# Kernel tuning notes

Hardware: AMD Instinct MI355X
Metric: run time of the kernel (lower is better)

Reference implementation:

```python
import jax, jax.numpy as jnp
import numpy as np

NUM_EMBEDDINGS = 8192
EMBEDDING_DIM = 128


def setup_inputs() -> dict:
    key = jax.random.key(0)
    k1, k2 = jax.random.split(key)
    inputs = jax.random.normal(k1, (8, 32, 32, EMBEDDING_DIM), dtype=jnp.float32)
    embedding_weight = jax.random.normal(k2, (NUM_EMBEDDINGS, EMBEDDING_DIM), dtype=jnp.float32)
    return {"inputs": inputs, "embedding_weight": embedding_weight}


def reference(inputs, embedding_weight):
    # inputs: [B, H, W, C] channels-last; embedding_weight: [K, C]
    input_shape = inputs.shape
    flat_input = inputs.reshape(-1, EMBEDDING_DIM)  # [N, C]

    distances = (
        jnp.sum(flat_input ** 2, axis=1, keepdims=True)
        + jnp.sum(embedding_weight ** 2, axis=1)
        - 2.0 * flat_input @ embedding_weight.T
    )
    encoding_indices = jnp.argmin(distances, axis=1)  # [N]

    # one-hot encodings (returned by the original module)
    encodings = jax.nn.one_hot(encoding_indices, NUM_EMBEDDINGS, dtype=jnp.float32)  # [N, K]

    # quantized via direct gather (same math as one_hot @ weight, no big matmul)
    quantized = embedding_weight[encoding_indices].reshape(input_shape)  # [B,H,W,C]

    # straight-through estimator
    quantized = inputs + jax.lax.stop_gradient(quantized - inputs)

    quantized_nchw = jnp.transpose(quantized, (0, 3, 1, 2))  # [B,C,H,W]
    return quantized_nchw, encodings
```

## Files before the change

kernel.cpp:

```cpp
#include <hip/hip_runtime.h>

typedef _Float16 f16x4 __attribute__((ext_vector_type(4)));
typedef _Float16 f16x8 __attribute__((ext_vector_type(8)));
typedef float    f32x16 __attribute__((ext_vector_type(16)));

#define HN_OFF   0u
#define BEST_OFF 32768u
#define ERH_OFF  98304u
#define ERL_OFF  (98304u + 2097152u)
#define XRH_OFF  (98304u + 2u * 2097152u)
#define XRL_OFF  (98304u + 3u * 2097152u)

#define OUT_Q    0
#define OUT_ENC  1048576

__global__ __launch_bounds__(256) void k1_convert(const float* __restrict__ x,
                                                  const float* __restrict__ e,
                                                  char* __restrict__ wsb) {
    int bx = blockIdx.x, tid = threadIdx.x;
    bool is_e = bx < 1024;
    const float* src = is_e ? e : x;
    int sec = is_e ? bx : bx - 1024;
    size_t off = (size_t)sec * 1024 + tid * 4;
    float4 v = *(const float4*)(src + off);

    f16x4 hi, lo;
    hi[0] = (_Float16)v.x; hi[1] = (_Float16)v.y;
    hi[2] = (_Float16)v.z; hi[3] = (_Float16)v.w;
    lo[0] = (_Float16)((v.x - (float)hi[0]) * 2048.0f);
    lo[1] = (_Float16)((v.y - (float)hi[1]) * 2048.0f);
    lo[2] = (_Float16)((v.z - (float)hi[2]) * 2048.0f);
    lo[3] = (_Float16)((v.w - (float)hi[3]) * 2048.0f);

    _Float16* ph = (_Float16*)(wsb + (is_e ? ERH_OFF : XRH_OFF));
    _Float16* pl = (_Float16*)(wsb + (is_e ? ERL_OFF : XRL_OFF));
    *(f16x4*)(ph + off) = hi;
    *(f16x4*)(pl + off) = lo;

    if (is_e) {
        float s = v.x * v.x + v.y * v.y + v.z * v.z + v.w * v.w;
        for (int o = 16; o > 0; o >>= 1) s += __shfl_down(s, o, 32);
        if ((tid & 31) == 0)
            ((float*)(wsb + HN_OFF))[off >> 7] = 0.5f * s;
    } else if (sec < 32) {
        ((unsigned long long*)(wsb + BEST_OFF))[sec * 256 + tid] = 0ull;
    }
}

__global__ __launch_bounds__(256, 2) void k2_mfma(char* __restrict__ wsb,
                                                  float* __restrict__ out) {
    __shared__ _Float16 lds_eh[128 * 128];
    __shared__ _Float16 lds_el[128 * 128];
    __shared__ float    lds_hn[1024];

    const _Float16* xrh = (const _Float16*)(wsb + XRH_OFF);
    const _Float16* xrl = (const _Float16*)(wsb + XRL_OFF);
    const _Float16* erh = (const _Float16*)(wsb + ERH_OFF);
    const _Float16* erl = (const _Float16*)(wsb + ERL_OFF);
    const float* hn = (const float*)(wsb + HN_OFF);
    unsigned long long* bestg = (unsigned long long*)(wsb + BEST_OFF);

    int tid = threadIdx.x;
    int lane = tid & 63, wave = tid >> 6;
    int col = lane & 31, half = lane >> 5;
    int bx = blockIdx.x, by = blockIdx.y;
    int r0 = bx * 128;
    int k0g = by * 1024;
    int row = r0 + wave * 32 + col;

    f16x8 ah[8], al[8];
    #pragma unroll
    for (int s = 0; s < 8; s++) {
        ah[s] = *(const f16x8*)(xrh + (size_t)row * 128 + s * 16 + half * 8);
        al[s] = *(const f16x8*)(xrl + (size_t)row * 128 + s * 16 + half * 8);
    }

    *(float4*)(lds_hn + tid * 4) = *(const float4*)(hn + k0g + tid * 4);

    float best[16];
    int bidx[16];
    #pragma unroll
    for (int i = 0; i < 16; i++) { best[i] = -3.0e38f; bidx[i] = 0; }

    float4* enc4 = (float4*)(out + OUT_ENC);
    long zb = (long)(by * 64 + bx) * 32768;
    float4 z4 = make_float4(0.f, 0.f, 0.f, 0.f);

    for (int kt = 0; kt < 8; kt++) {
        __syncthreads();
        #pragma unroll
        for (int i = 0; i < 16; i++) {
            int g = tid + i * 256;
            int gg = g & 2047;
            int code = gg >> 4, c16 = gg & 15;
            const _Float16* srcp = (i < 8) ? erh : erl;
            f16x8 v = *(const f16x8*)(srcp +
                         (size_t)(k0g + kt * 128 + code) * 128 + c16 * 8);
            _Float16* dstp = (i < 8) ? lds_eh : lds_el;
            *(f16x8*)(dstp + code * 128 + ((c16 ^ (code & 15)) * 8)) = v;
        }
        #pragma unroll
        for (int i = 0; i < 16; i++) enc4[zb + kt * 4096 + i * 256 + tid] = z4;
        __syncthreads();

        #pragma unroll
        for (int sub = 0; sub < 4; sub++) {
            f32x16 a0, a1, a2;
            #pragma unroll
            for (int i = 0; i < 16; i++) { a0[i] = 0.f; a1[i] = 0.f; a2[i] = 0.f; }
            int cbase = (sub * 32 + col) * 128;
            #pragma unroll
            for (int s = 0; s < 8; s++) {
                int so = ((s * 2 + half) ^ (col & 15)) * 8;
                f16x8 bh = *(const f16x8*)(lds_eh + cbase + so);
                f16x8 bl = *(const f16x8*)(lds_el + cbase + so);
                a0 = __builtin_amdgcn_mfma_f32_32x32x16_f16(ah[s], bh, a0, 0, 0, 0);
                a1 = __builtin_amdgcn_mfma_f32_32x32x16_f16(ah[s], bl, a1, 0, 0, 0);
                a2 = __builtin_amdgcn_mfma_f32_32x32x16_f16(al[s], bh, a2, 0, 0, 0);
            }
            int code = k0g + kt * 128 + sub * 32 + col;
            float hnv = lds_hn[kt * 128 + sub * 32 + col];
            #pragma unroll
            for (int r = 0; r < 16; r++) {
                float sc = a0[r] + (a1[r] + a2[r]) * (1.0f / 2048.0f) - hnv;
                if (sc > best[r]) { best[r] = sc; bidx[r] = code; }
            }
        }
    }

    #pragma unroll
    for (int r = 0; r < 16; r++) {
        float s = best[r];
        int bi = bidx[r];
        #pragma unroll
        for (int m = 1; m < 32; m <<= 1) {
            float qs = __shfl_xor(s, m, 64);
            int qi = __shfl_xor(bi, m, 64);
            if (qs > s || (qs == s && qi < bi)) { s = qs; bi = qi; }
        }
        if (col == 0) {
            int rl = (r & 3) + 8 * (r >> 2) + 4 * half;
            unsigned ub = __float_as_uint(s);
            ub = ((int)ub < 0) ? ~ub : (ub | 0x80000000u);
            unsigned long long p = ((unsigned long long)ub << 32) |
                                   (unsigned long long)(0xFFFFFFFFu - (unsigned)bi);
            atomicMax(&bestg[r0 + wave * 32 + rl], p);
        }
    }
}

__global__ __launch_bounds__(256) void k3_final(const char* __restrict__ wsb,
                                                const float* __restrict__ wgt,
                                                float* __restrict__ out) {
    int n = blockIdx.x * 256 + threadIdx.x;
    unsigned long long p = ((const unsigned long long*)(wsb + BEST_OFF))[n];
    int bi = (int)(0xFFFFFFFFu - (unsigned)(p & 0xFFFFFFFFull));

    out[(size_t)OUT_ENC + (size_t)n * 8192 + bi] = 1.0f;

    int bq = n >> 10, hw = n & 1023;
    float* o = out + (size_t)bq * 131072 + hw;
    const float4* wrow = (const float4*)(wgt + (size_t)bi * 128);
    #pragma unroll
    for (int c4 = 0; c4 < 32; c4++) {
        float4 v = wrow[c4];
        o[(c4 * 4 + 0) * 1024] = v.x;
        o[(c4 * 4 + 1) * 1024] = v.y;
        o[(c4 * 4 + 2) * 1024] = v.z;
        o[(c4 * 4 + 3) * 1024] = v.w;
    }
}

extern "C" void kernel_launch(void* const* d_in, const int* in_sizes, int n_in,
                              void* d_out, int out_size, void* d_ws, size_t ws_size,
                              hipStream_t stream) {
    const float* x = (const float*)d_in[0];
    const float* e = (const float*)d_in[1];
    float* out = (float*)d_out;
    char* ws = (char*)d_ws;

    k1_convert<<<2048, 256, 0, stream>>>(x, e, ws);
    k2_mfma<<<dim3(64, 8), 256, 0, stream>>>(ws, out);
    k3_final<<<32, 256, 0, stream>>>(ws, e, out);
}
```

Before: 328.4 us.

## Pre-swizzle codebook into MFMA fragment order and read B operands directly from global

The convert kernel now writes the fp16 hi/lo codebook planes in a layout that matches the MFMA B-fragment access pattern, using an LDS transpose per 128-code block. The main kernel then drops its LDS staging and both per-tile __syncthreads, loading B fragments straight from global/L2 and reading the half-norms from global. The aim is to remove LDS round-trips and barrier stalls, at the cost of more global/L2 traffic, since each wave re-fetches the codebook tile and loses LDS sharing across waves. The one-hot zero stores are moved after the compute of each tile.

```diff
diff --git a/kernel.cpp b/kernel.cpp
--- a/kernel.cpp
+++ b/kernel.cpp
@@ -6,57 +6,79 @@
 
 #define HN_OFF   0u
 #define BEST_OFF 32768u
-#define ERH_OFF  98304u
-#define ERL_OFF  (98304u + 2097152u)
+#define EFH_OFF  98304u
+#define EFL_OFF  (98304u + 2097152u)
 #define XRH_OFF  (98304u + 2u * 2097152u)
 #define XRL_OFF  (98304u + 3u * 2097152u)
 
-#define OUT_Q    0
 #define OUT_ENC  1048576
 
 __global__ __launch_bounds__(256) void k1_convert(const float* __restrict__ x,
                                                   const float* __restrict__ e,
                                                   char* __restrict__ wsb) {
     int bx = blockIdx.x, tid = threadIdx.x;
-    bool is_e = bx < 1024;
-    const float* src = is_e ? e : x;
-    int sec = is_e ? bx : bx - 1024;
-    size_t off = (size_t)sec * 1024 + tid * 4;
-    float4 v = *(const float4*)(src + off);
-
-    f16x4 hi, lo;
-    hi[0] = (_Float16)v.x; hi[1] = (_Float16)v.y;
-    hi[2] = (_Float16)v.z; hi[3] = (_Float16)v.w;
-    lo[0] = (_Float16)((v.x - (float)hi[0]) * 2048.0f);
-    lo[1] = (_Float16)((v.y - (float)hi[1]) * 2048.0f);
-    lo[2] = (_Float16)((v.z - (float)hi[2]) * 2048.0f);
-    lo[3] = (_Float16)((v.w - (float)hi[3]) * 2048.0f);
-
-    _Float16* ph = (_Float16*)(wsb + (is_e ? ERH_OFF : XRH_OFF));
-    _Float16* pl = (_Float16*)(wsb + (is_e ? ERL_OFF : XRL_OFF));
-    *(f16x4*)(ph + off) = hi;
-    *(f16x4*)(pl + off) = lo;
-
-    if (is_e) {
-        float s = v.x * v.x + v.y * v.y + v.z * v.z + v.w * v.w;
-        for (int o = 16; o > 0; o >>= 1) s += __shfl_down(s, o, 32);
-        if ((tid & 31) == 0)
-            ((float*)(wsb + HN_OFF))[off >> 7] = 0.5f * s;
-    } else if (sec < 32) {
-        ((unsigned long long*)(wsb + BEST_OFF))[sec * 256 + tid] = 0ull;
+    if (bx < 64) {
+        __shared__ f16x8 lds[4096];
+        const float* src = e + (size_t)bx * 16384;
+        float* hnp = (float*)(wsb + HN_OFF);
+        #pragma unroll
+        for (int it = 0; it < 8; it++) {
+            int g = it * 256 + tid;
+            int row = g >> 4, c16 = g & 15;
+            float4 v0 = *(const float4*)(src + row * 128 + c16 * 8);
+            float4 v1 = *(const float4*)(src + row * 128 + c16 * 8 + 4);
+            float f[8] = {v0.x, v0.y, v0.z, v0.w, v1.x, v1.y, v1.z, v1.w};
+            f16x8 hi, lo;
+            float ss = 0.f;
+            #pragma unroll
+            for (int j = 0; j < 8; j++) {
+                hi[j] = (_Float16)f[j];
+                lo[j] = (_Float16)((f[j] - (float)hi[j]) * 2048.0f);
+                ss += f[j] * f[j];
+            }
+            int sw = row ^ c16;
+            lds[c16 * 128 + sw] = hi;
+            lds[2048 + c16 * 128 + sw] = lo;
+            #pragma unroll
+            for (int o = 8; o > 0; o >>= 1) ss += __shfl_down(ss, o, 16);
+            if ((tid & 15) == 0) hnp[bx * 128 + row] = 0.5f * ss;
+        }
+        __syncthreads();
+        _Float16* eh = (_Float16*)(wsb + EFH_OFF);
+        _Float16* el = (_Float16*)(wsb + EFL_OFF);
+        #pragma unroll
+        for (int it = 0; it < 16; it++) {
+            int g = it * 256 + tid;
+            int plane = g >> 11, gg = g & 2047;
+            int chunk = gg >> 7, code = gg & 127;
+            f16x8 v = lds[plane * 2048 + chunk * 128 + (code ^ chunk)];
+            _Float16* dst = plane ? el : eh;
+            *(f16x8*)(dst + ((size_t)bx * 2048 + gg) * 8) = v;
+        }
+    } else {
+        int sec = bx - 64;
+        size_t off = (size_t)sec * 1024 + tid * 4;
+        float4 v = *(const float4*)(x + off);
+        f16x4 hi, lo;
+        hi[0] = (_Float16)v.x; hi[1] = (_Float16)v.y;
+        hi[2] = (_Float16)v.z; hi[3] = (_Float16)v.w;
+        lo[0] = (_Float16)((v.x - (float)hi[0]) * 2048.0f);
+        lo[1] = (_Float16)((v.y - (float)hi[1]) * 2048.0f);
+        lo[2] = (_Float16)((v.z - (float)hi[2]) * 2048.0f);
+        lo[3] = (_Float16)((v.w - (float)hi[3]) * 2048.0f);
+        *(f16x4*)((_Float16*)(wsb + XRH_OFF) + off) = hi;
+        *(f16x4*)((_Float16*)(wsb + XRL_OFF) + off) = lo;
+        if (sec < 32)
+            ((unsigned long long*)(wsb + BEST_OFF))[sec * 256 + tid] = 0ull;
     }
 }
 
 __global__ __launch_bounds__(256, 2) void k2_mfma(char* __restrict__ wsb,
                                                   float* __restrict__ out) {
-    __shared__ _Float16 lds_eh[128 * 128];
-    __shared__ _Float16 lds_el[128 * 128];
-    __shared__ float    lds_hn[1024];
-
     const _Float16* xrh = (const _Float16*)(wsb + XRH_OFF);
     const _Float16* xrl = (const _Float16*)(wsb + XRL_OFF);
-    const _Float16* erh = (const _Float16*)(wsb + ERH_OFF);
-    const _Float16* erl = (const _Float16*)(wsb + ERL_OFF);
+    const f16x8* efh = (const f16x8*)(wsb + EFH_OFF);
+    const f16x8* efl = (const f16x8*)(wsb + EFL_OFF);
     const float* hn = (const float*)(wsb + HN_OFF);
     unsigned long long* bestg = (unsigned long long*)(wsb + BEST_OFF);
 
@@ -75,8 +97,6 @@
         al[s] = *(const f16x8*)(xrl + (size_t)row * 128 + s * 16 + half * 8);
     }
 
-    *(float4*)(lds_hn + tid * 4) = *(const float4*)(hn + k0g + tid * 4);
-
     float best[16];
     int bidx[16];
     #pragma unroll
@@ -87,45 +107,31 @@
     float4 z4 = make_float4(0.f, 0.f, 0.f, 0.f);
 
     for (int kt = 0; kt < 8; kt++) {
-        __syncthreads();
-        #pragma unroll
-        for (int i = 0; i < 16; i++) {
-            int g = tid + i * 256;
-            int gg = g & 2047;
-            int code = gg >> 4, c16 = gg & 15;
-            const _Float16* srcp = (i < 8) ? erh : erl;
-            f16x8 v = *(const f16x8*)(srcp +
-                         (size_t)(k0g + kt * 128 + code) * 128 + c16 * 8);
-            _Float16* dstp = (i < 8) ? lds_eh : lds_el;
-            *(f16x8*)(dstp + code * 128 + ((c16 ^ (code & 15)) * 8)) = v;
-        }
-        #pragma unroll
-        for (int i = 0; i < 16; i++) enc4[zb + kt * 4096 + i * 256 + tid] = z4;
-        __syncthreads();
-
+        const f16x8* ebh = efh + ((size_t)(by * 8 + kt) * 2048 + half * 128 + col);
+        const f16x8* ebl = efl + ((size_t)(by * 8 + kt) * 2048 + half * 128 + col);
         #pragma unroll
         for (int sub = 0; sub < 4; sub++) {
+            float hnv = hn[k0g + kt * 128 + sub * 32 + col];
             f32x16 a0, a1, a2;
             #pragma unroll
             for (int i = 0; i < 16; i++) { a0[i] = 0.f; a1[i] = 0.f; a2[i] = 0.f; }
-            int cbase = (sub * 32 + col) * 128;
             #pragma unroll
             for (int s = 0; s < 8; s++) {
-                int so = ((s * 2 + half) ^ (col & 15)) * 8;
-                f16x8 bh = *(const f16x8*)(lds_eh + cbase + so);
-                f16x8 bl = *(const f16x8*)(lds_el + cbase + so);
+                f16x8 bh = ebh[s * 256 + sub * 32];
+                f16x8 bl = ebl[s * 256 + sub * 32];
                 a0 = __builtin_amdgcn_mfma_f32_32x32x16_f16(ah[s], bh, a0, 0, 0, 0);
                 a1 = __builtin_amdgcn_mfma_f32_32x32x16_f16(ah[s], bl, a1, 0, 0, 0);
                 a2 = __builtin_amdgcn_mfma_f32_32x32x16_f16(al[s], bh, a2, 0, 0, 0);
             }
             int code = k0g + kt * 128 + sub * 32 + col;
-            float hnv = lds_hn[kt * 128 + sub * 32 + col];
             #pragma unroll
             for (int r = 0; r < 16; r++) {
                 float sc = a0[r] + (a1[r] + a2[r]) * (1.0f / 2048.0f) - hnv;
                 if (sc > best[r]) { best[r] = sc; bidx[r] = code; }
             }
         }
+        #pragma unroll
+        for (int i = 0; i < 16; i++) enc4[zb + kt * 4096 + i * 256 + tid] = z4;
     }
 
     #pragma unroll
@@ -179,7 +185,7 @@
     float* out = (float*)d_out;
     char* ws = (char*)d_ws;
 
-    k1_convert<<<2048, 256, 0, stream>>>(x, e, ws);
+    k1_convert<<<1088, 256, 0, stream>>>(x, e, ws);
     k2_mfma<<<dim3(64, 8), 256, 0, stream>>>(ws, out);
     k3_final<<<32, 256, 0, stream>>>(ws, e, out);
 }
```

Result: slower. 349.7 us (+6.5%).
